# Kernel optimization log

Measured on AMD Instinct MI355X. Metric: run time of the kernel, lower is better.

## Reference

```python
import jax, jax.numpy as jnp
import numpy as np

VOCAB = 50000; EMBED = 300; KDIM = 128; KNUM = 21; KSIZES = (1, 2, 3)
B = 32; QLEN = 32; DLEN = 1024


def _kernel_mus(n):
    mus = [1.0]
    bs = 2.0 / (n - 1)
    mus.append(1.0 - bs / 2)
    for i in range(1, n - 1):
        mus.append(mus[i] - bs)
    return np.asarray(mus, np.float32)


def _kernel_sigmas(n):
    return np.asarray([0.001] + [0.1] * (n - 1), np.float32)


def setup_inputs() -> dict:
    key = jax.random.key(0)
    ks = jax.random.split(key, 12)
    inp = {
        'query_ids': jax.random.randint(ks[0], (B, QLEN), 0, VOCAB),
        'query_masks': jnp.ones((B, QLEN), jnp.float32),
        'doc_ids': jax.random.randint(ks[1], (B, DLEN), 0, VOCAB),
        'doc_masks': jnp.ones((B, DLEN), jnp.float32),
        'emb': jax.random.normal(ks[2], (VOCAB, EMBED), jnp.float32) * 0.02,
    }
    for i, k in enumerate(KSIZES):
        inp[f'conv_w{i+1}'] = jax.random.normal(ks[3 + i], (KDIM, EMBED, k), jnp.float32) / np.sqrt(EMBED * k)
        inp[f'conv_b{i+1}'] = jnp.zeros((KDIM,), jnp.float32)
    feat = KNUM * len(KSIZES) ** 2  # 189
    inp['dense_w'] = jax.random.normal(ks[9], (feat, 1), jnp.float32) * 0.05
    inp['dense_b'] = jnp.zeros((1,), jnp.float32)
    return inp


def _conv_relu(x, w, b):
    # x: [B, L, E], w: [O, E, K] -> [B, L-K+1, O] (VALID conv, matches torch Conv1d no padding)
    y = jax.lax.conv_general_dilated(x, w, (1,), 'VALID', dimension_numbers=('NWC', 'OIW', 'NWC'))
    return jax.nn.relu(y + b)


def _matcher(k_enc, k_mask, v_enc, v_mask, mus, sig):
    kn = k_enc / (jnp.linalg.norm(k_enc, axis=-1, keepdims=True) + 1e-13)
    vn = v_enc / (jnp.linalg.norm(v_enc, axis=-1, keepdims=True) + 1e-13)
    inter = jnp.einsum('bqd,bvd->bqv', kn, vn) * (k_mask[:, :, None] * v_mask[:, None, :])
    # multi-Gaussian soft-histogram over similarity: [B, q, v, KNUM]
    ko = jnp.exp(-((inter[..., None] - mus) ** 2) / (2.0 * sig ** 2))
    kde = jnp.log(jnp.maximum(ko.sum(axis=2), 1e-10)) * 0.01  # [B, q, KNUM]
    return (kde * k_mask[..., None]).sum(axis=1)  # [B, KNUM]


def reference(query_ids, query_masks, doc_ids, doc_masks, emb,
              conv_w1, conv_b1, conv_w2, conv_b2, conv_w3, conv_b3,
              dense_w, dense_b):
    mus = jnp.asarray(_kernel_mus(KNUM))
    sig = jnp.asarray(_kernel_sigmas(KNUM))
    qe = emb[query_ids]  # [B, QLEN, E]
    de = emb[doc_ids]    # [B, DLEN, E]
    cw = [(conv_w1, conv_b1), (conv_w2, conv_b2), (conv_w3, conv_b3)]
    q_encs = [_conv_relu(qe, w, b) for w, b in cw]
    d_encs = [_conv_relu(de, w, b) for w, b in cw]
    logits = jnp.concatenate([
        _matcher(q, query_masks[:, :q.shape[1]], d, doc_masks[:, :d.shape[1]], mus, sig)
        for q in q_encs for d in d_encs], axis=1)  # [B, 189]
    score = (logits @ dense_w + dense_b).squeeze(-1)  # [B]
    return score, logits
```

## Files before the change

kernel.cpp:

```cpp
#include <hip/hip_runtime.h>
#include <hip/hip_bf16.h>
#include <math.h>

#define NB 32
#define QL 32
#define DL 1024
#define EMB 300
#define EMBP 320
#define OD 128
#define KNUM 21
#define VOCAB 50000

typedef short short8 __attribute__((ext_vector_type(8)));
typedef float floatx4 __attribute__((ext_vector_type(4)));

static const size_t WP_OFF  = 0;
static const size_t DPK_OFF = 122880;
static const size_t QPK_OFF = 5365760;
static const size_t QH_OFF  = 5529920;
static const size_t QLO_OFF = 5726528;
static const size_t DH_OFF  = 5923136;
static const size_t DLO_OFF = 12214592;
static const size_t ACC_OFF = 18506048;
static const int ACC_SZ = 9 * NB * QL * KNUM;

#define QPLANE 131072
#define DPLANE 4194304

#define MROWS (NB * DL + NB * QL)
#define MTILES 264
#define CONV_BLOCKS (MTILES * 3)

__device__ __constant__ int WPOFF_C[3] = {0, 40960, 122880};

__device__ __forceinline__ void gl_lds16(const ushort* g, char* l) {
    __builtin_amdgcn_global_load_lds(
        (const __attribute__((address_space(1))) unsigned int*)(g),
        (__attribute__((address_space(3))) unsigned int*)(l), 16, 0, 0);
}

__device__ __forceinline__ ushort bf16_bits(float f) {
    __hip_bfloat16 h = __float2bfloat16(f);
    return *reinterpret_cast<ushort*>(&h);
}

__global__ void prep_w_kernel(const float* __restrict__ w1,
                              const float* __restrict__ w2,
                              const float* __restrict__ w3,
                              ushort* __restrict__ wp) {
    int idx = blockIdx.x * 256 + threadIdx.x;
    if (idx >= 245760) return;
    const float* src;
    int k, rel, base;
    if (idx < 40960)        { k = 1; rel = idx;          src = w1; base = 0; }
    else if (idx < 122880)  { k = 2; rel = idx - 40960;  src = w2; base = 40960; }
    else                    { k = 3; rel = idx - 122880; src = w3; base = 122880; }
    int kd = 320 * k;
    int o = rel / kd;
    int jc = rel - o * kd;
    int j = jc / EMBP;
    int c = jc - j * EMBP;
    float f = (c < EMB) ? src[(o * EMB + c) * k + j] : 0.f;
    wp[base + rel] = bf16_bits(f);
}

__global__ void gather_pack(const float* __restrict__ emb,
                            const int* __restrict__ dids, const int* __restrict__ qids,
                            ushort* __restrict__ dpk, ushort* __restrict__ qpk) {
    int idx = blockIdx.x * 256 + threadIdx.x;
    const int DROWS = NB * DL;
    if (idx >= (DROWS + NB * QL + 2) * 40) return;
    int r = idx / 40;
    int c0 = (idx - r * 40) * 8;
    int rid;
    ushort* dst;
    if (r < DROWS) { rid = dids[r]; dst = dpk + (size_t)r * EMBP; }
    else if (r < DROWS + NB * QL) { rid = qids[r - DROWS]; dst = qpk + (size_t)(r - DROWS) * EMBP; }
    else {
        uint4 zz = {0u, 0u, 0u, 0u};
        *reinterpret_cast<uint4*>(qpk + (size_t)(r - DROWS) * EMBP + c0) = zz;
        return;
    }
    const float* erow = emb + (size_t)rid * EMB;
    ushort v[8];
    if (c0 + 8 <= EMB) {
        float4 f0 = *reinterpret_cast<const float4*>(erow + c0);
        float4 f1 = *reinterpret_cast<const float4*>(erow + c0 + 4);
        float fv[8] = {f0.x, f0.y, f0.z, f0.w, f1.x, f1.y, f1.z, f1.w};
#pragma unroll
        for (int i = 0; i < 8; ++i) v[i] = bf16_bits(fv[i]);
    } else {
#pragma unroll
        for (int i = 0; i < 8; ++i) {
            int c = c0 + i;
            v[i] = bf16_bits((c < EMB) ? erow[c] : 0.f);
        }
    }
    *reinterpret_cast<uint4*>(dst + c0) = *reinterpret_cast<uint4*>(v);
}

__global__ __launch_bounds__(256) void conv_mfma(const ushort* __restrict__ xpk,
                                                 const float* __restrict__ dmask,
                                                 const float* __restrict__ qmask,
                                                 const ushort* __restrict__ wp,
                                                 const float* __restrict__ b1,
                                                 const float* __restrict__ b2,
                                                 const float* __restrict__ b3,
                                                 ushort* __restrict__ dh,
                                                 ushort* __restrict__ dlo,
                                                 ushort* __restrict__ qh,
                                                 ushort* __restrict__ qlo) {
    __shared__ __align__(16) char smem[2][33024];

    const int tid = threadIdx.x;
    const int bid = blockIdx.x;
    const int swz = (bid & 7) * (CONV_BLOCKS / 8) + (bid >> 3);
    const int z = swz % 3;
    const int tile = swz / 3;
    const int l0 = tile * 128;

    const int Kdim = EMBP * (z + 1);
    const int nk = 5 * (z + 1);
    const ushort* wpk = wp + WPOFF_C[z];
    const float* bias = (z == 0) ? b1 : ((z == 1) ? b2 : b3);

    const int wave = tid >> 6;
    const int lane = tid & 63;
    const int l15 = lane & 15;
    const int quad = lane >> 4;
    const int wm = wave >> 1;
    const int wn = wave & 1;

    const int srow = lane >> 3;
    const int scol = (lane & 7) * 8;
    const ushort* a0 = xpk + (size_t)(l0 + wave * 8 + srow) * EMBP + scol;
    const ushort* at = xpk + (size_t)(l0 + 128 + srow) * EMBP + scol;
    const ushort* b0 = wpk + (size_t)(wave * 8 + srow) * Kdim + scol;

    auto stage = [&](int buf, int kk) {
        int jj = (kk >= 10) ? 2 : ((kk >= 5) ? 1 : 0);
        int coff = (kk - jj * 5) * 64;
        int koff = kk * 64;
        char* abuf = smem[buf];
        char* bbuf = smem[buf] + 16640;
#pragma unroll
        for (int p = 0; p < 4; ++p)
            gl_lds16(a0 + p * (32 * EMBP) + coff, abuf + p * 4096 + wave * 1024);
        if (wave == 0 && lane < 16)
            gl_lds16(at + coff, abuf + 16384);
#pragma unroll
        for (int p = 0; p < 4; ++p)
            gl_lds16(b0 + (size_t)p * 32 * Kdim + koff, bbuf + p * 4096 + wave * 1024);
    };

    floatx4 acc[4][4];
#pragma unroll
    for (int i = 0; i < 4; ++i)
#pragma unroll
        for (int j = 0; j < 4; ++j) acc[i][j] = (floatx4)0.f;

    stage(0, 0);
    __syncthreads();

    int jjc = 0, ccc = 0;
    int buf = 0;
    for (int kk = 0; kk < nk; ++kk) {
        if (kk + 1 < nk) stage(buf ^ 1, kk + 1);
        const char* Ab = smem[buf];
        const char* Bb = smem[buf] + 16640;
        short8 af[2][4], bf[2][4];
#pragma unroll
        for (int h = 0; h < 2; ++h)
#pragma unroll
            for (int i = 0; i < 4; ++i) {
                af[h][i] = *reinterpret_cast<const short8*>(
                    Ab + (wm * 64 + i * 16 + l15 + jjc) * 128 + h * 64 + quad * 16);
                bf[h][i] = *reinterpret_cast<const short8*>(
                    Bb + (wn * 64 + i * 16 + l15) * 128 + h * 64 + quad * 16);
            }
#pragma unroll
        for (int h = 0; h < 2; ++h)
#pragma unroll
            for (int i = 0; i < 4; ++i)
#pragma unroll
                for (int j = 0; j < 4; ++j)
                    acc[i][j] = __builtin_amdgcn_mfma_f32_16x16x32_bf16(af[h][i], bf[h][j], acc[i][j], 0, 0, 0);
        ++ccc;
        if (ccc == 5) { ccc = 0; ++jjc; }
        __syncthreads();
        buf ^= 1;
    }

    float (*rowsum)[128] = reinterpret_cast<float(*)[128]>(smem);
    float bv[4];
#pragma unroll
    for (int j = 0; j < 4; ++j) bv[j] = bias[wn * 64 + j * 16 + l15];
#pragma unroll
    for (int i = 0; i < 4; ++i)
#pragma unroll
        for (int r = 0; r < 4; ++r) {
            float p = 0.f;
#pragma unroll
            for (int j = 0; j < 4; ++j) {
                float y = fmaxf(acc[i][j][r] + bv[j], 0.f);
                acc[i][j][r] = y;
                p += y * y;
            }
#pragma unroll
            for (int m = 1; m < 16; m <<= 1) p += __shfl_xor(p, m, 64);
            if (l15 == 0) rowsum[wn][wm * 64 + i * 16 + quad * 4 + r] = p;
        }
    __syncthreads();

#pragma unroll
    for (int i = 0; i < 4; ++i) {
#pragma unroll
        for (int rr = 0; rr < 4; ++rr) {
            int rl = wm * 64 + i * 16 + quad * 4 + rr;
            int r = l0 + rl;
            float tot = rowsum[0][rl] + rowsum[1][rl];
            float mv;
            ushort* hp;
            ushort* lp;
            if (r < NB * DL) {
                int l = r & (DL - 1);
                if (l >= DL - z) continue;
                mv = dmask[r];
                size_t base = (size_t)z * DPLANE + (size_t)r * OD;
                hp = dh + base; lp = dlo + base;
            } else {
                int t = r - NB * DL;
                int l = t & (QL - 1);
                if (l >= QL - z) continue;
                mv = qmask[t];
                size_t base = (size_t)z * QPLANE + (size_t)t * OD;
                hp = qh + base; lp = qlo + base;
            }
            float sc = mv / (sqrtf(tot) + 1e-13f);
            int cb = wn * 64 + l15;
#pragma unroll
            for (int j = 0; j < 4; ++j) {
                float v = acc[i][j][rr] * sc;
                __hip_bfloat16 h = __float2bfloat16(v);
                float hf = __bfloat162float(h);
                hp[cb + j * 16] = *reinterpret_cast<ushort*>(&h);
                __hip_bfloat16 l = __float2bfloat16(v - hf);
                lp[cb + j * 16] = *reinterpret_cast<ushort*>(&l);
            }
        }
    }
}

__global__ __launch_bounds__(256) void matcher_kernel(const ushort* __restrict__ qh_g,
                                                      const ushort* __restrict__ ql_g,
                                                      const ushort* __restrict__ vh_g,
                                                      const ushort* __restrict__ vl_g,
                                                      float* __restrict__ accb) {
    __shared__ __align__(16) float Sm[32 * 132];

    const int tid = threadIdx.x;
    const int pp = blockIdx.z;
    const int b = blockIdx.y;
    const int v0 = blockIdx.x * 128;
    const int qi = pp / 3;
    const int di = pp - qi * 3;
    const int Vk = 1024 - di;

    const ushort* qhb = qh_g + (size_t)qi * QPLANE + (size_t)b * (QL * OD);
    const ushort* qlb = ql_g + (size_t)qi * QPLANE + (size_t)b * (QL * OD);
    const ushort* vhb = vh_g + (size_t)di * DPLANE + (size_t)b * (DL * OD) + (size_t)v0 * OD;
    const ushort* vlb = vl_g + (size_t)di * DPLANE + (size_t)b * (DL * OD) + (size_t)v0 * OD;

    const int wave = tid >> 6;
    const int lane = tid & 63;
    const int l15 = lane & 15;
    const int quad = lane >> 4;

    floatx4 acc[2][2];
#pragma unroll
    for (int i = 0; i < 2; ++i)
#pragma unroll
        for (int j = 0; j < 2; ++j) acc[i][j] = (floatx4)0.f;

#pragma unroll
    for (int kw = 0; kw < 4; ++kw) {
        const int ko = kw * 32 + quad * 8;
        short8 qh[2], ql[2], vh[2], vl[2];
#pragma unroll
        for (int i = 0; i < 2; ++i) {
            const int qr = i * 16 + l15;
            const int vr = wave * 32 + i * 16 + l15;
            qh[i] = *reinterpret_cast<const short8*>(qhb + qr * OD + ko);
            ql[i] = *reinterpret_cast<const short8*>(qlb + qr * OD + ko);
            vh[i] = *reinterpret_cast<const short8*>(vhb + (size_t)vr * OD + ko);
            vl[i] = *reinterpret_cast<const short8*>(vlb + (size_t)vr * OD + ko);
        }
#pragma unroll
        for (int i = 0; i < 2; ++i)
#pragma unroll
            for (int j = 0; j < 2; ++j) {
                acc[i][j] = __builtin_amdgcn_mfma_f32_16x16x32_bf16(qh[i], vh[j], acc[i][j], 0, 0, 0);
                acc[i][j] = __builtin_amdgcn_mfma_f32_16x16x32_bf16(qh[i], vl[j], acc[i][j], 0, 0, 0);
                acc[i][j] = __builtin_amdgcn_mfma_f32_16x16x32_bf16(ql[i], vh[j], acc[i][j], 0, 0, 0);
            }
    }

    const int vmax = min(128, Vk - v0);
#pragma unroll
    for (int i = 0; i < 2; ++i)
#pragma unroll
        for (int j = 0; j < 2; ++j)
#pragma unroll
            for (int r = 0; r < 4; ++r) {
                int q = i * 16 + quad * 4 + r;
                int v = wave * 32 + j * 16 + l15;
                float val = acc[i][j][r];
                if (v >= vmax) val = 1.0e4f;
                Sm[q * 132 + v] = val;
            }
    __syncthreads();

    for (int idx = tid; idx < 32 * KNUM; idx += 256) {
        int q = idx & 31;
        int t = idx >> 5;
        float mu = (t == 0) ? 1.0f : 0.95f - 0.1f * (float)(t - 1);
        float Am = (t == 0) ? -721347.52f : -72.13475204f;
        const float* srow = &Sm[q * 132];
        float a0 = 0.f, a1 = 0.f, a2 = 0.f, a3 = 0.f;
#pragma unroll 8
        for (int j = 0; j < 32; ++j) {
            float4 s4 = *reinterpret_cast<const float4*>(&srow[4 * j]);
            float d0 = s4.x - mu;
            float d1 = s4.y - mu;
            float d2 = s4.z - mu;
            float d3 = s4.w - mu;
            a0 += __builtin_exp2f(Am * d0 * d0);
            a1 += __builtin_exp2f(Am * d1 * d1);
            a2 += __builtin_exp2f(Am * d2 * d2);
            a3 += __builtin_exp2f(Am * d3 * d3);
        }
        atomicAdd(&accb[((pp * NB + b) * QL + q) * KNUM + t], (a0 + a1) + (a2 + a3));
    }
}

__global__ void finalize_kernel(const float* __restrict__ accb,
                                const float* __restrict__ qmask,
                                const float* __restrict__ dw,
                                const float* __restrict__ db,
                                float* __restrict__ out) {
    __shared__ float prod[192];
    int b = blockIdx.x;
    int tid = threadIdx.x;
    if (tid < 189) {
        int pq = tid / 21;
        int t = tid - pq * 21;
        int qi = pq / 3;
        int Qk = 32 - qi;
        const float* ab = accb + ((pq * NB + b) * QL) * KNUM + t;
        float s = 0.f;
        for (int q = 0; q < Qk; ++q)
            s += logf(fmaxf(ab[q * KNUM], 1e-10f)) * qmask[b * QL + q];
        float lg = s * 0.01f;
        out[NB + b * 189 + tid] = lg;
        prod[tid] = lg * dw[tid];
    }
    __syncthreads();
    if (tid == 0) {
        float sc = db[0];
        for (int i = 0; i < 189; ++i) sc += prod[i];
        out[b] = sc;
    }
}

extern "C" void kernel_launch(void* const* d_in, const int* in_sizes, int n_in,
                              void* d_out, int out_size, void* d_ws, size_t ws_size,
                              hipStream_t stream) {
    const int* qids = (const int*)d_in[0];
    const float* qmask = (const float*)d_in[1];
    const int* dids = (const int*)d_in[2];
    const float* dmask = (const float*)d_in[3];
    const float* emb = (const float*)d_in[4];
    const float* w1 = (const float*)d_in[5];
    const float* b1 = (const float*)d_in[6];
    const float* w2 = (const float*)d_in[7];
    const float* b2 = (const float*)d_in[8];
    const float* w3 = (const float*)d_in[9];
    const float* b3 = (const float*)d_in[10];
    const float* dw = (const float*)d_in[11];
    const float* db = (const float*)d_in[12];
    float* out = (float*)d_out;
    float* ws = (float*)d_ws;

    ushort* wp  = (ushort*)(ws + WP_OFF);
    ushort* dpk = (ushort*)(ws + DPK_OFF);
    ushort* qpk = (ushort*)(ws + QPK_OFF);
    ushort* qh  = (ushort*)(ws + QH_OFF);
    ushort* qlo = (ushort*)(ws + QLO_OFF);
    ushort* dh  = (ushort*)(ws + DH_OFF);
    ushort* dlo = (ushort*)(ws + DLO_OFF);
    float* accb = ws + ACC_OFF;

    hipMemsetAsync(accb, 0, ACC_SZ * sizeof(float), stream);
    prep_w_kernel<<<960, 256, 0, stream>>>(w1, w2, w3, wp);
    gather_pack<<<((MROWS + 2) * 40 + 255) / 256, 256, 0, stream>>>(emb, dids, qids, dpk, qpk);

    conv_mfma<<<CONV_BLOCKS, 256, 0, stream>>>(dpk, dmask, qmask, wp, b1, b2, b3, dh, dlo, qh, qlo);

    matcher_kernel<<<dim3(8, NB, 9), 256, 0, stream>>>(qh, qlo, dh, dlo, accb);
    finalize_kernel<<<NB, 256, 0, stream>>>(accb, qmask, dw, db, out);
}
```

Baseline: 254.5 us.

## Compute Gaussian kernel bins by recurrence instead of per-bin exponentials

Replaces the per-(q, bin) loop that evaluated 21 exponentials per similarity with a per-thread loop over 16 similarities. For evenly spaced mus it derives all 20 sigma=0.1 bins from one exp2 seed, one ratio exp2 and constant factors, then combines partial bins with lane shuffles before the atomics. This cuts transcendental work about tenfold. The exp2 seed is offset by 2^126 and rescaled to avoid underflow, so accuracy for far-away bins depends on the chained multiplies.

```diff
diff --git a/kernel.cpp b/kernel.cpp
--- a/kernel.cpp
+++ b/kernel.cpp
@@ -320,26 +320,66 @@
             }
     __syncthreads();
 
-    for (int idx = tid; idx < 32 * KNUM; idx += 256) {
-        int q = idx & 31;
-        int t = idx >> 5;
-        float mu = (t == 0) ? 1.0f : 0.95f - 0.1f * (float)(t - 1);
-        float Am = (t == 0) ? -721347.52f : -72.13475204f;
-        const float* srow = &Sm[q * 132];
-        float a0 = 0.f, a1 = 0.f, a2 = 0.f, a3 = 0.f;
-#pragma unroll 8
-        for (int j = 0; j < 32; ++j) {
-            float4 s4 = *reinterpret_cast<const float4*>(&srow[4 * j]);
-            float d0 = s4.x - mu;
-            float d1 = s4.y - mu;
-            float d2 = s4.z - mu;
-            float d3 = s4.w - mu;
-            a0 += __builtin_exp2f(Am * d0 * d0);
-            a1 += __builtin_exp2f(Am * d1 * d1);
-            a2 += __builtin_exp2f(Am * d2 * d2);
-            a3 += __builtin_exp2f(Am * d3 * d3);
-        }
-        atomicAdd(&accb[((pp * NB + b) * QL + q) * KNUM + t], (a0 + a1) + (a2 + a3));
+    {
+        const int q = tid >> 3;
+        const int c = tid & 7;
+        const float* srow = &Sm[q * 132 + c * 16];
+        const float Am  = -72.13475204f;
+        const float Am5 = -14.426950408f;
+        const float A0  = -721347.52f;
+        const float C   = 0x1.0p-126f;
+        const float G[19] = {
+            6.0653066e-01f, 2.2313016e-01f, 8.2084999e-02f, 3.0197383e-02f,
+            1.1108997e-02f, 4.0867714e-03f, 1.5034391e-03f, 5.5308438e-04f,
+            2.0346837e-04f, 7.4851830e-05f, 2.7536450e-05f, 1.0130095e-05f,
+            3.7266532e-06f, 1.3709590e-06f, 5.0434766e-07f, 1.8553914e-07f,
+            6.8256033e-08f, 2.5110699e-08f, 9.2374496e-09f};
+
+        float bins[21];
+#pragma unroll
+        for (int t = 0; t < 21; ++t) bins[t] = 0.f;
+
+#pragma unroll
+        for (int jj = 0; jj < 4; ++jj) {
+            float4 s4 = *reinterpret_cast<const float4*>(srow + jj * 4);
+            float sv[4] = {s4.x, s4.y, s4.z, s4.w};
+            float tp[4], R[4];
+#pragma unroll
+            for (int e = 0; e < 4; ++e) {
+                float d1 = sv[e] - 0.95f;
+                tp[e] = __builtin_exp2f(__builtin_fmaf(Am * d1, d1, 126.f));
+                R[e]  = __builtin_exp2f(Am5 * d1);
+                bins[1] = __builtin_fmaf(tp[e], C, bins[1]);
+            }
+#pragma unroll
+            for (int t = 2; t <= 20; ++t) {
+                const float g = G[t - 2];
+#pragma unroll
+                for (int e = 0; e < 4; ++e) {
+                    tp[e] *= R[e] * g;
+                    bins[t] = __builtin_fmaf(tp[e], C, bins[t]);
+                }
+            }
+#pragma unroll
+            for (int e = 0; e < 4; ++e) {
+                float d0 = sv[e] - 1.0f;
+                bins[0] += __builtin_exp2f((A0 * d0) * d0);
+            }
+        }
+
+#pragma unroll
+        for (int t = 0; t < 21; ++t) {
+            float v = bins[t];
+            v += __shfl_xor(v, 1, 64);
+            v += __shfl_xor(v, 2, 64);
+            v += __shfl_xor(v, 4, 64);
+            bins[t] = v;
+        }
+        if (c == 0) {
+            float* dst = &accb[((pp * NB + b) * QL + q) * KNUM];
+#pragma unroll
+            for (int t = 0; t < 21; ++t) atomicAdd(dst + t, bins[t]);
+        }
     }
 }
 
```

Measured after the change: 303.0 us. 19.0% more time.

## Compute Gaussian kernel bins by geometric recurrence instead of per-bin exp

Applied to the files above, without the earlier changes.

Replaces the per-(q,kernel) loop that evaluated one exp2 per similarity per kernel with a per-(q,column-chunk) loop. Each thread computes one Gaussian value and one ratio exponential per similarity, then derives the other 19 kernels by multiplying with precomputed constant factors. The intent is to cut transcendental instruction count roughly tenfold in the soft-histogram stage. To avoid underflow it scales values by 2^126 and multiplies back. It adds a shuffle reduction across 8 lanes and 21 atomics per row. This risks precision loss and denormal or overflow issues for far-off bins.

```diff
diff --git a/kernel.cpp b/kernel.cpp
--- a/kernel.cpp
+++ b/kernel.cpp
@@ -320,26 +320,71 @@
             }
     __syncthreads();
 
-    for (int idx = tid; idx < 32 * KNUM; idx += 256) {
-        int q = idx & 31;
-        int t = idx >> 5;
-        float mu = (t == 0) ? 1.0f : 0.95f - 0.1f * (float)(t - 1);
-        float Am = (t == 0) ? -721347.52f : -72.13475204f;
-        const float* srow = &Sm[q * 132];
-        float a0 = 0.f, a1 = 0.f, a2 = 0.f, a3 = 0.f;
-#pragma unroll 8
-        for (int j = 0; j < 32; ++j) {
-            float4 s4 = *reinterpret_cast<const float4*>(&srow[4 * j]);
-            float d0 = s4.x - mu;
-            float d1 = s4.y - mu;
-            float d2 = s4.z - mu;
-            float d3 = s4.w - mu;
-            a0 += __builtin_exp2f(Am * d0 * d0);
-            a1 += __builtin_exp2f(Am * d1 * d1);
-            a2 += __builtin_exp2f(Am * d2 * d2);
-            a3 += __builtin_exp2f(Am * d3 * d3);
-        }
-        atomicAdd(&accb[((pp * NB + b) * QL + q) * KNUM + t], (a0 + a1) + (a2 + a3));
+    {
+        const int q = tid >> 3;
+        const int c = tid & 7;
+        const float* srow = &Sm[q * 132 + c * 16];
+        const float Am  = -72.13475204f;
+        const float Am5 = -14.426950408f;
+        const float A0  = -721347.52f;
+        const float C   = 0x1.0p-126f;
+
+        float s00 = 0.f, s01 = 0.f, s02 = 0.f, s03 = 0.f, s04 = 0.f, s05 = 0.f,
+              s06 = 0.f, s07 = 0.f, s08 = 0.f, s09 = 0.f, s10 = 0.f, s11 = 0.f,
+              s12 = 0.f, s13 = 0.f, s14 = 0.f, s15 = 0.f, s16 = 0.f, s17 = 0.f,
+              s18 = 0.f, s19 = 0.f, s20 = 0.f;
+
+#define GACC(B) { B = __builtin_fmaf(tx, C, B); B = __builtin_fmaf(ty, C, B); \
+                  B = __builtin_fmaf(tz, C, B); B = __builtin_fmaf(tw, C, B); }
+#define GSTEP(B, g) { tx *= Rx * (g); ty *= Ry * (g); tz *= Rz * (g); tw *= Rw * (g); GACC(B) }
+
+#pragma unroll
+        for (int jj = 0; jj < 4; ++jj) {
+            float4 s4 = *reinterpret_cast<const float4*>(srow + jj * 4);
+            float dx = s4.x - 0.95f, dy = s4.y - 0.95f, dz = s4.z - 0.95f, dw = s4.w - 0.95f;
+            float tx = __builtin_exp2f(__builtin_fmaf(Am * dx, dx, 126.f));
+            float ty = __builtin_exp2f(__builtin_fmaf(Am * dy, dy, 126.f));
+            float tz = __builtin_exp2f(__builtin_fmaf(Am * dz, dz, 126.f));
+            float tw = __builtin_exp2f(__builtin_fmaf(Am * dw, dw, 126.f));
+            float Rx = __builtin_exp2f(Am5 * dx);
+            float Ry = __builtin_exp2f(Am5 * dy);
+            float Rz = __builtin_exp2f(Am5 * dz);
+            float Rw = __builtin_exp2f(Am5 * dw);
+            GACC(s01)
+            GSTEP(s02, 6.0653066e-01f) GSTEP(s03, 2.2313016e-01f)
+            GSTEP(s04, 8.2084999e-02f) GSTEP(s05, 3.0197383e-02f)
+            GSTEP(s06, 1.1108997e-02f) GSTEP(s07, 4.0867714e-03f)
+            GSTEP(s08, 1.5034391e-03f) GSTEP(s09, 5.5308438e-04f)
+            GSTEP(s10, 2.0346837e-04f) GSTEP(s11, 7.4851830e-05f)
+            GSTEP(s12, 2.7536450e-05f) GSTEP(s13, 1.0130095e-05f)
+            GSTEP(s14, 3.7266532e-06f) GSTEP(s15, 1.3709590e-06f)
+            GSTEP(s16, 5.0434766e-07f) GSTEP(s17, 1.8553914e-07f)
+            GSTEP(s18, 6.8256033e-08f) GSTEP(s19, 2.5110699e-08f)
+            GSTEP(s20, 9.2374496e-09f)
+            float ex = s4.x - 1.f, ey = s4.y - 1.f, ez = s4.z - 1.f, ew = s4.w - 1.f;
+            s00 += __builtin_exp2f((A0 * ex) * ex);
+            s00 += __builtin_exp2f((A0 * ey) * ey);
+            s00 += __builtin_exp2f((A0 * ez) * ez);
+            s00 += __builtin_exp2f((A0 * ew) * ew);
+        }
+#undef GSTEP
+#undef GACC
+
+#define GRED(B) { B += __shfl_xor(B, 1, 64); B += __shfl_xor(B, 2, 64); B += __shfl_xor(B, 4, 64); }
+        GRED(s00) GRED(s01) GRED(s02) GRED(s03) GRED(s04) GRED(s05) GRED(s06)
+        GRED(s07) GRED(s08) GRED(s09) GRED(s10) GRED(s11) GRED(s12) GRED(s13)
+        GRED(s14) GRED(s15) GRED(s16) GRED(s17) GRED(s18) GRED(s19) GRED(s20)
+#undef GRED
+        if (c == 0) {
+            float* dst = &accb[((pp * NB + b) * QL + q) * KNUM];
+            atomicAdd(dst + 0,  s00); atomicAdd(dst + 1,  s01); atomicAdd(dst + 2,  s02);
+            atomicAdd(dst + 3,  s03); atomicAdd(dst + 4,  s04); atomicAdd(dst + 5,  s05);
+            atomicAdd(dst + 6,  s06); atomicAdd(dst + 7,  s07); atomicAdd(dst + 8,  s08);
+            atomicAdd(dst + 9,  s09); atomicAdd(dst + 10, s10); atomicAdd(dst + 11, s11);
+            atomicAdd(dst + 12, s12); atomicAdd(dst + 13, s13); atomicAdd(dst + 14, s14);
+            atomicAdd(dst + 15, s15); atomicAdd(dst + 16, s16); atomicAdd(dst + 17, s17);
+            atomicAdd(dst + 18, s18); atomicAdd(dst + 19, s19); atomicAdd(dst + 20, s20);
+        }
     }
 }
 
```

After: 303.1 us. 1.19x slower.
